# Kernel tuning notes

Hardware: AMD Instinct MI355X
Metric: run time of the kernel (lower is better)

## Reference

```python
import jax, jax.numpy as jnp
import numpy as np

ADMP = 16  # admp_channel


def _backbone(x, Wc, bc):
    # Conv2d(3->256, k=3, stride=2, pad=1) + ReLU stands in for feature_backbone
    y = jax.lax.conv_general_dilated(x, Wc, window_strides=(2, 2),
                                     padding=((1, 1), (1, 1)),
                                     dimension_numbers=('NCHW', 'OIHW', 'NCHW'))
    return jax.nn.relu(y + bc[None, :, None, None])


def _feature_select(feat, k):
    # AdaptiveMaxPool2d(k, return_indices=True) on feat.sum(1); H,W divisible by k
    B, C, H, W = feat.shape
    bh, bw = H // k, W // k
    resp = feat.sum(1)  # [B,H,W]
    r = resp.reshape(B, k, bh, k, bw).transpose(0, 1, 3, 2, 4).reshape(B, k, k, bh * bw)
    loc = jnp.argmax(r, axis=-1)            # local flat index in each bh*bw block
    lr, lc = loc // bw, loc % bw
    rows = jnp.arange(k)[None, :, None] * bh + lr   # [B,k,k]
    cols = jnp.arange(k)[None, None, :] * bw + lc
    return (rows * W + cols).reshape(B, k * k)      # flat indices into H*W


def _mlp(x, W1, b1, W2, b2):
    # Linear -> ReLU -> (Dropout eval = identity) -> Linear
    return jax.nn.relu(x @ W1 + b1) @ W2 + b2


def reference(xA, xB, Wconv, bconv, W1r, b1r, W2r, b2r, W1c, b1c, W2c, b2c):
    fA = _backbone(xA, Wconv, bconv)  # [B,C,H,W]
    fB = _backbone(xB, Wconv, bconv)
    B, C, H, W = fA.shape
    N = H * W
    idxA = _feature_select(fA, ADMP)                       # [B,K]
    fA_flat = fA.reshape(B, C, N)
    fB_flat = fB.reshape(B, C, N)
    desc = jnp.take_along_axis(fA_flat, idxA[:, None, :], axis=2)  # [B,C,K]
    # ||a-b||^2 = ||a||^2 - 2 a.b + ||b||^2 ; fused batched kNN
    dist = ((desc ** 2).sum(1)[:, :, None]
            - 2.0 * jnp.einsum('bck,bcn->bkn', desc, fB_flat)
            + (fB_flat ** 2).sum(1)[:, None, :])           # [B,K,N]
    minidx = jnp.argmin(dist, axis=-1)                     # [B,K]
    # original uses high (==width here since H==W) for both div and mod
    row_A, col_A = idxA // H, idxA % H
    row_B, col_B = minidx // H, minidx % H
    drow = (row_B - row_A).astype(jnp.float32)             # [B,K]
    dcol = (col_A - col_B).astype(jnp.float32)
    out_drow = _mlp(drow, W1r, b1r, W2r, b2r)              # [B,1]
    out_dcol = _mlp(dcol, W1c, b1c, W2c, b2c)
    return jnp.concatenate([out_drow, out_dcol], axis=1)   # [B,2]


def setup_inputs() -> dict:
    key = jax.random.key(0)
    ks = jax.random.split(key, 8)
    K2 = ADMP * ADMP
    return {
        'xA': jax.random.normal(ks[0], (4, 3, 256, 256), jnp.float32),
        'xB': jax.random.normal(ks[1], (4, 3, 256, 256), jnp.float32),
        'Wconv': jax.random.normal(ks[2], (256, 3, 3, 3), jnp.float32) * 0.1,
        'bconv': jnp.zeros((256,), jnp.float32),
        'W1r': jax.random.normal(ks[3], (K2, K2 // 2), jnp.float32) * 0.05,
        'b1r': jnp.zeros((K2 // 2,), jnp.float32),
        'W2r': jax.random.normal(ks[4], (K2 // 2, 1), jnp.float32) * 0.05,
        'b2r': jnp.zeros((1,), jnp.float32),
        'W1c': jax.random.normal(ks[5], (K2, K2 // 2), jnp.float32) * 0.05,
        'b1c': jnp.zeros((K2 // 2,), jnp.float32),
        'W2c': jax.random.normal(ks[6], (K2 // 2, 1), jnp.float32) * 0.05,
        'b2c': jnp.zeros((1,), jnp.float32),
    }
```

## Files before the change

### kernel.cpp

```cpp
#include <hip/hip_runtime.h>
#include <stdint.h>

constexpr int NB   = 4;
constexpr int CIN  = 3;
constexpr int HIN  = 256;
constexpr int COUT = 256;
constexpr int HF   = 128;
constexpr int NF   = HF * HF;
constexpr int KADM = 16;
constexpr int KK   = KADM * KADM;
constexpr int HID  = 128;
constexpr int DFB  = 65536;
constexpr int PX   = 64;
constexpr int NT   = NF / PX;

typedef unsigned short ushort_t;
typedef __attribute__((ext_vector_type(8))) _Float16 f16x8;
typedef __attribute__((ext_vector_type(2))) __fp16   fp16v2;
typedef __attribute__((ext_vector_type(4))) float    f32x4;

__device__ inline ushort_t f16bits(_Float16 h) { return __builtin_bit_cast(ushort_t, h); }

__device__ inline int swz(int pix, int c) {
    return pix * 256 + ((((c >> 3) ^ (pix & 7)) << 3) | (c & 7));
}

__device__ inline int dfoff(int kt, int chunk, int lane) {
    return ((kt * 8 + chunk) * 64 + lane) * 8;
}

__global__ __launch_bounds__(256) void prep_kernel(
        const float* __restrict__ W, ushort_t* __restrict__ WFh, ushort_t* __restrict__ WFl)
{
    int co = threadIdx.x;
    int kt = co >> 4, la = co & 15;
    #pragma unroll
    for (int q = 0; q < 32; ++q) {
        float v = (q < 27) ? W[co * 27 + q] : 0.f;
        _Float16 h = (_Float16)v;
        _Float16 l = (_Float16)(v - (float)h);
        int lg = q >> 3, e = q & 7;
        int off = (kt * 64 + lg * 16 + la) * 8 + e;
        WFh[off] = f16bits(h);
        WFl[off] = f16bits(l);
    }
}

__global__ __launch_bounds__(256) void convA_kernel(
        const float* __restrict__ xA,
        const ushort_t* __restrict__ WFh, const ushort_t* __restrict__ WFl,
        const float* __restrict__ bias, float* __restrict__ resp)
{
    __shared__ float    pS[CIN][3][132];
    __shared__ ushort_t Ah[64][40];
    __shared__ ushort_t Al[64][40];
    __shared__ float    redS[4][64];

    int tile = blockIdx.x;
    int b    = blockIdx.y;
    int oh   = tile >> 1;
    int ow0  = (tile & 1) << 6;
    const float* x = xA + (size_t)b * CIN * HIN * HIN;
    int tid = threadIdx.x;

    for (int i = tid; i < CIN * 3 * 129; i += 256) {
        int ci = i / (3 * 129);
        int r2 = i % (3 * 129);
        int kh = r2 / 129, c = r2 % 129;
        int gr = 2 * oh - 1 + kh, gc = 2 * ow0 - 1 + c;
        float v = 0.f;
        if (gr >= 0 && gr < HIN && gc >= 0 && gc < HIN)
            v = x[(size_t)ci * HIN * HIN + (size_t)gr * HIN + gc];
        pS[ci][kh][c] = v;
    }
    __syncthreads();

    {
        int n = tid >> 2, qg = tid & 3;
        unsigned uh[4], ul[4];
        #pragma unroll
        for (int e2 = 0; e2 < 4; ++e2) {
            ushort_t hh[2], ll[2];
            #pragma unroll
            for (int s = 0; s < 2; ++s) {
                int q = qg * 8 + e2 * 2 + s;
                float v = 0.f;
                if (q < 27) {
                    int ci = q / 9, r = (q % 9) / 3, kw = q % 3;
                    v = pS[ci][r][2 * n + kw];
                }
                _Float16 h = (_Float16)v;
                _Float16 l = (_Float16)(v - (float)h);
                hh[s] = f16bits(h); ll[s] = f16bits(l);
            }
            uh[e2] = (unsigned)hh[0] | ((unsigned)hh[1] << 16);
            ul[e2] = (unsigned)ll[0] | ((unsigned)ll[1] << 16);
        }
        *(uint4*)&Ah[n][qg * 8] = *(uint4*)uh;
        *(uint4*)&Al[n][qg * 8] = *(uint4*)ul;
    }
    __syncthreads();

    int lane = tid & 63, w = tid >> 6;
    int la = lane & 15, lg = lane >> 4;
    int wbase = w * 64;

    float bj[4];
    f16x8 bh[4], bl[4];
    #pragma unroll
    for (int j = 0; j < 4; ++j) {
        bj[j] = bias[wbase + j * 16 + la];
        int off = ((w * 4 + j) * 64 + lane) * 8;
        bh[j] = *(const f16x8*)&WFh[off];
        bl[j] = *(const f16x8*)&WFl[off];
    }

    f16x8 ah[4], al[4];
    #pragma unroll
    for (int i = 0; i < 4; ++i) {
        ah[i] = *(const f16x8*)&Ah[i * 16 + la][lg * 8];
        al[i] = *(const f16x8*)&Al[i * 16 + la][lg * 8];
    }

    f32x4 acc[4][4];
    #pragma unroll
    for (int i = 0; i < 4; ++i)
        #pragma unroll
        for (int j = 0; j < 4; ++j) acc[i][j] = (f32x4)0.f;

    #pragma unroll
    for (int i = 0; i < 4; ++i)
        #pragma unroll
        for (int j = 0; j < 4; ++j) {
            acc[i][j] = __builtin_amdgcn_mfma_f32_16x16x32_f16(ah[i], bh[j], acc[i][j], 0, 0, 0);
            acc[i][j] = __builtin_amdgcn_mfma_f32_16x16x32_f16(al[i], bh[j], acc[i][j], 0, 0, 0);
            acc[i][j] = __builtin_amdgcn_mfma_f32_16x16x32_f16(ah[i], bl[j], acc[i][j], 0, 0, 0);
        }

    float s[4][4];
    #pragma unroll
    for (int i = 0; i < 4; ++i)
        #pragma unroll
        for (int r = 0; r < 4; ++r) s[i][r] = 0.f;

    #pragma unroll
    for (int i = 0; i < 4; ++i)
        #pragma unroll
        for (int j = 0; j < 4; ++j)
            #pragma unroll
            for (int r = 0; r < 4; ++r)
                s[i][r] += fmaxf(acc[i][j][r] + bj[j], 0.f);

    #pragma unroll
    for (int i = 0; i < 4; ++i)
        #pragma unroll
        for (int r = 0; r < 4; ++r) {
            float v = s[i][r];
            v += __shfl_xor(v, 1, 64);
            v += __shfl_xor(v, 2, 64);
            v += __shfl_xor(v, 4, 64);
            v += __shfl_xor(v, 8, 64);
            s[i][r] = v;
        }
    if (la == 0) {
        #pragma unroll
        for (int i = 0; i < 4; ++i)
            #pragma unroll
            for (int r = 0; r < 4; ++r)
                redS[w][i * 16 + lg * 4 + r] = s[i][r];
    }
    __syncthreads();
    if (tid < 64) {
        float tot = redS[0][tid] + redS[1][tid] + redS[2][tid] + redS[3][tid];
        resp[(size_t)b * NF + oh * HF + ow0 + tid] = tot;
    }
}

__global__ __launch_bounds__(256) void select_kernel(
        const float* __restrict__ resp,
        const float* __restrict__ xA, const float* __restrict__ W,
        const float* __restrict__ bias,
        int* __restrict__ idxA,
        ushort_t* __restrict__ dFh, ushort_t* __restrict__ dFl,
        float* __restrict__ normA)
{
    __shared__ float patch[27];
    __shared__ float red[4];
    __shared__ int   sidx;

    int bk = blockIdx.x;
    int b = bk >> 8, k = bk & 255;
    int t = threadIdx.x;

    if (t < 64) {
        int kr = k >> 4, kc = k & 15;
        int lr = t >> 3, lc = t & 7;
        int row = kr * 8 + lr, col = kc * 8 + lc;
        float bv = resp[(size_t)b * NF + (size_t)row * HF + col];
        int best = t;
        for (int off = 32; off > 0; off >>= 1) {
            float ov = __shfl_down(bv, off, 64);
            int   oi = __shfl_down(best, off, 64);
            if (ov > bv || (ov == bv && oi < best)) { bv = ov; best = oi; }
        }
        if (t == 0) {
            int r = kr * 8 + (best >> 3), c = kc * 8 + (best & 7);
            int idx = r * HF + c;
            idxA[bk] = idx;
            sidx = idx;
        }
    }
    __syncthreads();
    int idx = sidx;
    int oh = idx >> 7, ow = idx & 127;

    if (t < 27) {
        int ci = t / 9, kh = (t % 9) / 3, kw = t % 3;
        int ir = oh * 2 - 1 + kh, ic = ow * 2 - 1 + kw;
        float v = 0.f;
        if (ir >= 0 && ir < HIN && ic >= 0 && ic < HIN)
            v = xA[((size_t)b * CIN + ci) * HIN * HIN + (size_t)ir * HIN + ic];
        patch[t] = v;
    }
    __syncthreads();

    float v = bias[t];
    const float* w = &W[t * 27];
    #pragma unroll
    for (int q = 0; q < 27; ++q) v = fmaf(patch[q], w[q], v);
    v = fmaxf(v, 0.f);

    _Float16 h = (_Float16)v;
    _Float16 l = (_Float16)(v - (float)h);
    {
        int kt = k >> 4, la = k & 15;
        int chunk = t >> 5, lg = (t >> 3) & 3, e = t & 7;
        int off = b * DFB + dfoff(kt, chunk, lg * 16 + la) + e;
        dFh[off] = f16bits(h);
        dFl[off] = f16bits(l);
    }

    float s = v * v;
    for (int off = 32; off > 0; off >>= 1) s += __shfl_down(s, off, 64);
    if ((t & 63) == 0) red[t >> 6] = s;
    __syncthreads();
    if (t == 0) normA[bk] = red[0] + red[1] + red[2] + red[3];
}

__device__ inline void load_desc(const ushort_t* __restrict__ dFh,
                                 const ushort_t* __restrict__ dFl,
                                 int w, int chunk, int lane,
                                 f16x8* bh, f16x8* bl)
{
    #pragma unroll
    for (int jj = 0; jj < 2; ++jj) {
        int off = dfoff(w * 2 + jj, chunk, lane);
        bh[jj] = *(const f16x8*)&dFh[off];
        bl[jj] = *(const f16x8*)&dFl[off];
    }
}

__device__ inline void knn_chunk(const ushort_t* __restrict__ fH,
                                 const ushort_t* __restrict__ fL,
                                 int la, int lg, int cc,
                                 const f16x8* bh, const f16x8* bl,
                                 f32x4 (&acc)[4][2])
{
    #pragma unroll
    for (int i = 0; i < 4; ++i) {
        f16x8 ah = *(const f16x8*)&fH[swz(i * 16 + la, cc + lg * 8)];
        f16x8 al = *(const f16x8*)&fL[swz(i * 16 + la, cc + lg * 8)];
        __builtin_amdgcn_s_setprio(1);
        #pragma unroll
        for (int jj = 0; jj < 2; ++jj) {
            acc[i][jj] = __builtin_amdgcn_mfma_f32_16x16x32_f16(ah, bh[jj], acc[i][jj], 0, 0, 0);
            acc[i][jj] = __builtin_amdgcn_mfma_f32_16x16x32_f16(al, bh[jj], acc[i][jj], 0, 0, 0);
            acc[i][jj] = __builtin_amdgcn_mfma_f32_16x16x32_f16(ah, bl[jj], acc[i][jj], 0, 0, 0);
        }
        __builtin_amdgcn_s_setprio(0);
    }
}

__global__ __launch_bounds__(512, 4) void fused_kernel(
        const float* __restrict__ xB,
        const ushort_t* __restrict__ WFh, const ushort_t* __restrict__ WFl,
        const float* __restrict__ bias,
        const ushort_t* __restrict__ dFhg, const ushort_t* __restrict__ dFlg,
        const float* __restrict__ normA,
        unsigned long long* __restrict__ packed)
{
    __shared__ __align__(16) char smem[2 * PX * 256 * 2];
    __shared__ float redS[8][PX];
    __shared__ float nAS[KK];
    __shared__ float nBS[PX];
    __shared__ float bS[COUT];

    float*    pSp = (float*)smem;
    ushort_t* AhP = (ushort_t*)(smem + 4752);
    ushort_t* AlP = (ushort_t*)(smem + 4752 + 5120);
    ushort_t* fH  = (ushort_t*)smem;
    ushort_t* fL  = (ushort_t*)(smem + PX * 256 * 2);

    int tile = blockIdx.x;
    int b    = blockIdx.y;
    int oh   = tile >> 1;
    int ow0  = (tile & 1) << 6;
    const float* x = xB + (size_t)b * CIN * HIN * HIN;
    int tid = threadIdx.x;

    if (tid < KK) {
        nAS[tid] = normA[b * KK + tid];
        bS[tid]  = bias[tid];
    }

    for (int i = tid; i < CIN * 3 * 129; i += 512) {
        int ci = i / (3 * 129);
        int r2 = i % (3 * 129);
        int kh = r2 / 129, c = r2 % 129;
        int gr = 2 * oh - 1 + kh, gc = 2 * ow0 - 1 + c;
        float v = 0.f;
        if (gr >= 0 && gr < HIN && gc >= 0 && gc < HIN)
            v = x[(size_t)ci * HIN * HIN + (size_t)gr * HIN + gc];
        pSp[ci * 396 + kh * 132 + c] = v;
    }
    __syncthreads();

    {
        int n = tid >> 3, qg = tid & 7;
        ushort_t hh[4], ll[4];
        #pragma unroll
        for (int s = 0; s < 4; ++s) {
            int q = qg * 4 + s;
            float v = 0.f;
            if (q < 27) {
                int ci = q / 9, r = (q % 9) / 3, kw = q % 3;
                v = pSp[ci * 396 + r * 132 + 2 * n + kw];
            }
            _Float16 h = (_Float16)v;
            _Float16 l = (_Float16)(v - (float)h);
            hh[s] = f16bits(h); ll[s] = f16bits(l);
        }
        unsigned lo, hi;
        lo = (unsigned)hh[0] | ((unsigned)hh[1] << 16);
        hi = (unsigned)hh[2] | ((unsigned)hh[3] << 16);
        *(uint2*)&AhP[n * 40 + qg * 4] = make_uint2(lo, hi);
        lo = (unsigned)ll[0] | ((unsigned)ll[1] << 16);
        hi = (unsigned)ll[2] | ((unsigned)ll[3] << 16);
        *(uint2*)&AlP[n * 40 + qg * 4] = make_uint2(lo, hi);
    }
    __syncthreads();

    int lane = tid & 63, w = tid >> 6;
    int la = lane & 15, lg = lane >> 4;

    f16x8 wah[2], wal[2], pbh[4], pbl[4];
    #pragma unroll
    for (int jj = 0; jj < 2; ++jj) {
        int off = ((w * 2 + jj) * 64 + lane) * 8;
        wah[jj] = *(const f16x8*)&WFh[off];
        wal[jj] = *(const f16x8*)&WFl[off];
    }
    #pragma unroll
    for (int i = 0; i < 4; ++i) {
        pbh[i] = *(const f16x8*)&AhP[(i * 16 + la) * 40 + lg * 8];
        pbl[i] = *(const f16x8*)&AlP[(i * 16 + la) * 40 + lg * 8];
    }

    f32x4 cacc[2][4];
    #pragma unroll
    for (int jj = 0; jj < 2; ++jj)
        #pragma unroll
        for (int i = 0; i < 4; ++i) cacc[jj][i] = (f32x4)0.f;

    #pragma unroll
    for (int jj = 0; jj < 2; ++jj)
        #pragma unroll
        for (int i = 0; i < 4; ++i) {
            cacc[jj][i] = __builtin_amdgcn_mfma_f32_16x16x32_f16(wah[jj], pbh[i], cacc[jj][i], 0, 0, 0);
            cacc[jj][i] = __builtin_amdgcn_mfma_f32_16x16x32_f16(wal[jj], pbh[i], cacc[jj][i], 0, 0, 0);
            cacc[jj][i] = __builtin_amdgcn_mfma_f32_16x16x32_f16(wah[jj], pbl[i], cacc[jj][i], 0, 0, 0);
        }

    __syncthreads();

    float s2[4] = {0.f, 0.f, 0.f, 0.f};
    #pragma unroll
    for (int jj = 0; jj < 2; ++jj) {
        int co4 = (w * 2 + jj) * 16 + lg * 4;
        f32x4 b4 = *(const f32x4*)&bS[co4];
        int chunk = co4 >> 3;
        int within = (lg & 1) * 4;
        #pragma unroll
        for (int i = 0; i < 4; ++i) {
            int pix = i * 16 + la;
            float v0 = fmaxf(cacc[jj][i][0] + b4[0], 0.f);
            float v1 = fmaxf(cacc[jj][i][1] + b4[1], 0.f);
            float v2 = fmaxf(cacc[jj][i][2] + b4[2], 0.f);
            float v3 = fmaxf(cacc[jj][i][3] + b4[3], 0.f);
            s2[i] += v0 * v0 + v1 * v1 + v2 * v2 + v3 * v3;
            fp16v2 h01 = __builtin_amdgcn_cvt_pkrtz(v0, v1);
            fp16v2 h23 = __builtin_amdgcn_cvt_pkrtz(v2, v3);
            fp16v2 l01 = __builtin_amdgcn_cvt_pkrtz(v0 - (float)h01[0], v1 - (float)h01[1]);
            fp16v2 l23 = __builtin_amdgcn_cvt_pkrtz(v2 - (float)h23[0], v3 - (float)h23[1]);
            int base = pix * 256 + ((chunk ^ (pix & 7)) << 3) + within;
            *(uint2*)&fH[base] = make_uint2(__builtin_bit_cast(unsigned, h01),
                                            __builtin_bit_cast(unsigned, h23));
            *(uint2*)&fL[base] = make_uint2(__builtin_bit_cast(unsigned, l01),
                                            __builtin_bit_cast(unsigned, l23));
        }
    }

    const ushort_t* dFh = dFhg + (size_t)b * DFB;
    const ushort_t* dFl = dFlg + (size_t)b * DFB;
    f16x8 bhA[2], blA[2], bhB[2], blB[2];
    load_desc(dFh, dFl, w, 0, lane, bhA, blA);
    load_desc(dFh, dFl, w, 1, lane, bhB, blB);

    #pragma unroll
    for (int i = 0; i < 4; ++i) {
        float v = s2[i];
        v += __shfl_xor(v, 16, 64);
        v += __shfl_xor(v, 32, 64);
        if (lg == 0) redS[w][i * 16 + la] = v;
    }
    __syncthreads();
    if (tid < PX) {
        float t0 = 0.f;
        #pragma unroll
        for (int p = 0; p < 8; ++p) t0 += redS[p][tid];
        nBS[tid] = t0;
    }
    __syncthreads();

    f32x4 acc[4][2];
    #pragma unroll
    for (int i = 0; i < 4; ++i)
        #pragma unroll
        for (int jj = 0; jj < 2; ++jj) acc[i][jj] = (f32x4)0.f;

    knn_chunk(fH, fL, la, lg, 0, bhA, blA, acc);
    load_desc(dFh, dFl, w, 2, lane, bhA, blA);
    knn_chunk(fH, fL, la, lg, 32, bhB, blB, acc);
    load_desc(dFh, dFl, w, 3, lane, bhB, blB);
    knn_chunk(fH, fL, la, lg, 64, bhA, blA, acc);
    load_desc(dFh, dFl, w, 4, lane, bhA, blA);
    knn_chunk(fH, fL, la, lg, 96, bhB, blB, acc);
    load_desc(dFh, dFl, w, 5, lane, bhB, blB);
    knn_chunk(fH, fL, la, lg, 128, bhA, blA, acc);
    load_desc(dFh, dFl, w, 6, lane, bhA, blA);
    knn_chunk(fH, fL, la, lg, 160, bhB, blB, acc);
    load_desc(dFh, dFl, w, 7, lane, bhB, blB);
    knn_chunk(fH, fL, la, lg, 192, bhA, blA, acc);
    knn_chunk(fH, fL, la, lg, 224, bhB, blB, acc);

    float nBv[4][4];
    #pragma unroll
    for (int i = 0; i < 4; ++i) {
        f32x4 t4 = *(const f32x4*)&nBS[i * 16 + lg * 4];
        nBv[i][0] = t4[0]; nBv[i][1] = t4[1]; nBv[i][2] = t4[2]; nBv[i][3] = t4[3];
    }
    int n0 = tile * PX;
    float bd[2];
    int   bn[2];
    #pragma unroll
    for (int jj = 0; jj < 2; ++jj) {
        int kl = (w * 2 + jj) * 16 + la;
        float nAv = nAS[kl];
        float bestd = 3.4e38f;
        int   bestn = 0;
        #pragma unroll
        for (int i = 0; i < 4; ++i)
            #pragma unroll
            for (int r = 0; r < 4; ++r) {
                int n = n0 + i * 16 + lg * 4 + r;
                float d = fmaf(-2.f, acc[i][jj][r], nAv) + nBv[i][r];
                if (d < bestd) { bestd = d; bestn = n; }
            }
        #pragma unroll
        for (int off = 16; off <= 32; off <<= 1) {
            float od = __shfl_xor(bestd, off, 64);
            int   on = __shfl_xor(bestn, off, 64);
            bool take = (od < bestd) || (od == bestd && on < bestn);
            bestd = take ? od : bestd;
            bestn = take ? on : bestn;
        }
        bd[jj] = bestd; bn[jj] = bestn;
    }
    if (lg < 2) {
        float fd = (lg == 0) ? bd[0] : bd[1];
        int   fn = (lg == 0) ? bn[0] : bn[1];
        unsigned u = __float_as_uint(fd);
        u = (u & 0x80000000u) ? ~u : (u | 0x80000000u);
        unsigned long long key = ((unsigned long long)u << 32) | (unsigned)fn;
        int klw = (w * 2 + lg) * 16 + la;
        atomicMin(&packed[b * KK + klw], key);
    }
}

__global__ __launch_bounds__(128) void mlp_kernel(
        const int* __restrict__ idxA, const unsigned long long* __restrict__ packed,
        const float* __restrict__ W1r, const float* __restrict__ b1r,
        const float* __restrict__ W2r, const float* __restrict__ b2r,
        const float* __restrict__ W1c, const float* __restrict__ b1c,
        const float* __restrict__ W2c, const float* __restrict__ b2c,
        float* __restrict__ out)
{
    __shared__ float xS[KK];
    __shared__ float red[2];
    int blk = blockIdx.x;
    int b = blk >> 1, which = blk & 1;
    int t = threadIdx.x;

    for (int k = t; k < KK; k += 128) {
        int ia = idxA[b * KK + k];
        int nn = (int)(packed[b * KK + k] & 0xffffffffULL);
        int rowA = ia >> 7, colA = ia & 127;
        int rowB = nn >> 7, colB = nn & 127;
        xS[k] = (which == 0) ? (float)(rowB - rowA) : (float)(colA - colB);
    }
    __syncthreads();

    const float* W1 = which ? W1c : W1r;
    const float* b1 = which ? b1c : b1r;
    const float* W2 = which ? W2c : W2r;
    const float* b2 = which ? b2c : b2r;

    float h = b1[t];
    for (int k = 0; k < KK; ++k) h = fmaf(xS[k], W1[k * HID + t], h);
    h = fmaxf(h, 0.f);
    float pv = h * W2[t];
    for (int off = 32; off > 0; off >>= 1) pv += __shfl_down(pv, off, 64);
    if ((t & 63) == 0) red[t >> 6] = pv;
    __syncthreads();
    if (t == 0) out[b * 2 + which] = red[0] + red[1] + b2[0];
}

extern "C" void kernel_launch(void* const* d_in, const int* in_sizes, int n_in,
                              void* d_out, int out_size, void* d_ws, size_t ws_size,
                              hipStream_t stream)
{
    const float* xA  = (const float*)d_in[0];
    const float* xB  = (const float*)d_in[1];
    const float* Wc  = (const float*)d_in[2];
    const float* bc  = (const float*)d_in[3];
    const float* W1r = (const float*)d_in[4];
    const float* b1r = (const float*)d_in[5];
    const float* W2r = (const float*)d_in[6];
    const float* b2r = (const float*)d_in[7];
    const float* W1c = (const float*)d_in[8];
    const float* b1c = (const float*)d_in[9];
    const float* W2c = (const float*)d_in[10];
    const float* b2c = (const float*)d_in[11];
    float* out = (float*)d_out;

    char* ws = (char*)d_ws;
    unsigned long long* packed = (unsigned long long*)ws; ws += (size_t)NB * KK * 8;
    int*   idxA   = (int*)ws;      ws += (size_t)NB * KK * 4;
    float* normA  = (float*)ws;    ws += (size_t)NB * KK * 4;
    float* resp   = (float*)ws;    ws += (size_t)NB * NF * 4;
    ushort_t* dFh = (ushort_t*)ws; ws += (size_t)NB * DFB * 2;
    ushort_t* dFl = (ushort_t*)ws; ws += (size_t)NB * DFB * 2;
    ushort_t* WFh = (ushort_t*)ws; ws += (size_t)COUT * 32 * 2;
    ushort_t* WFl = (ushort_t*)ws; ws += (size_t)COUT * 32 * 2;

    hipMemsetAsync(packed, 0xFF, (size_t)NB * KK * 8, stream);

    prep_kernel  <<<1, 256, 0, stream>>>(Wc, WFh, WFl);
    convA_kernel <<<dim3(256, NB), 256, 0, stream>>>(xA, WFh, WFl, bc, resp);
    select_kernel<<<NB * KK, 256, 0, stream>>>(resp, xA, Wc, bc, idxA, dFh, dFl, normA);
    fused_kernel <<<dim3(NT, NB), 512, 0, stream>>>(xB, WFh, WFl, bc, dFh, dFl,
                                                    normA, packed);
    mlp_kernel   <<<8, 128, 0, stream>>>(idxA, packed,
                                         W1r, b1r, W2r, b2r,
                                         W1c, b1c, W2c, b2c, out);
}
```

Baseline: 60.26 us.

## Widen fused conv+kNN tile to full 128-pixel row with 1024-thread blocks

Each fused block now processes a full output row of 128 pixels using 16 waves, and each wave owns 16 descriptor columns instead of 32. The patch staging covers the full input row width, and the per-wave accumulators are reorganised as 8 pixel subtiles by 1 descriptor tile. This halves the block count and the per-block redundant loads of descriptors, norms and bias, and gives one atomic per descriptor per block. In exchange it doubles the shared memory per block and uses larger blocks, which may reduce occupancy or leave the GPU underfilled, since only 512 blocks are launched.

```diff
diff --git a/kernel.cpp b/kernel.cpp
--- a/kernel.cpp
+++ b/kernel.cpp
@@ -11,7 +11,7 @@
 constexpr int KK   = KADM * KADM;
 constexpr int HID  = 128;
 constexpr int DFB  = 65536;
-constexpr int PX   = 64;
+constexpr int PX   = 128;
 constexpr int NT   = NF / PX;
 
 typedef unsigned short ushort_t;
@@ -249,39 +249,33 @@
 
 __device__ inline void load_desc(const ushort_t* __restrict__ dFh,
                                  const ushort_t* __restrict__ dFl,
-                                 int w, int chunk, int lane,
-                                 f16x8* bh, f16x8* bl)
-{
-    #pragma unroll
-    for (int jj = 0; jj < 2; ++jj) {
-        int off = dfoff(w * 2 + jj, chunk, lane);
-        bh[jj] = *(const f16x8*)&dFh[off];
-        bl[jj] = *(const f16x8*)&dFl[off];
-    }
+                                 int kt, int chunk, int lane,
+                                 f16x8& bh, f16x8& bl)
+{
+    int off = dfoff(kt, chunk, lane);
+    bh = *(const f16x8*)&dFh[off];
+    bl = *(const f16x8*)&dFl[off];
 }
 
 __device__ inline void knn_chunk(const ushort_t* __restrict__ fH,
                                  const ushort_t* __restrict__ fL,
                                  int la, int lg, int cc,
-                                 const f16x8* bh, const f16x8* bl,
-                                 f32x4 (&acc)[4][2])
-{
-    #pragma unroll
-    for (int i = 0; i < 4; ++i) {
+                                 f16x8 bh, f16x8 bl,
+                                 f32x4 (&acc)[8])
+{
+    #pragma unroll
+    for (int i = 0; i < 8; ++i) {
         f16x8 ah = *(const f16x8*)&fH[swz(i * 16 + la, cc + lg * 8)];
         f16x8 al = *(const f16x8*)&fL[swz(i * 16 + la, cc + lg * 8)];
         __builtin_amdgcn_s_setprio(1);
-        #pragma unroll
-        for (int jj = 0; jj < 2; ++jj) {
-            acc[i][jj] = __builtin_amdgcn_mfma_f32_16x16x32_f16(ah, bh[jj], acc[i][jj], 0, 0, 0);
-            acc[i][jj] = __builtin_amdgcn_mfma_f32_16x16x32_f16(al, bh[jj], acc[i][jj], 0, 0, 0);
-            acc[i][jj] = __builtin_amdgcn_mfma_f32_16x16x32_f16(ah, bl[jj], acc[i][jj], 0, 0, 0);
-        }
+        acc[i] = __builtin_amdgcn_mfma_f32_16x16x32_f16(ah, bh, acc[i], 0, 0, 0);
+        acc[i] = __builtin_amdgcn_mfma_f32_16x16x32_f16(al, bh, acc[i], 0, 0, 0);
+        acc[i] = __builtin_amdgcn_mfma_f32_16x16x32_f16(ah, bl, acc[i], 0, 0, 0);
         __builtin_amdgcn_s_setprio(0);
     }
 }
 
-__global__ __launch_bounds__(512, 4) void fused_kernel(
+__global__ __launch_bounds__(1024, 4) void fused_kernel(
         const float* __restrict__ xB,
         const ushort_t* __restrict__ WFh, const ushort_t* __restrict__ WFl,
         const float* __restrict__ bias,
@@ -290,21 +284,19 @@
         unsigned long long* __restrict__ packed)
 {
     __shared__ __align__(16) char smem[2 * PX * 256 * 2];
-    __shared__ float redS[8][PX];
+    __shared__ float redS[16][PX];
     __shared__ float nAS[KK];
     __shared__ float nBS[PX];
     __shared__ float bS[COUT];
 
     float*    pSp = (float*)smem;
-    ushort_t* AhP = (ushort_t*)(smem + 4752);
-    ushort_t* AlP = (ushort_t*)(smem + 4752 + 5120);
+    ushort_t* AhP = (ushort_t*)(smem + 9360);
+    ushort_t* AlP = (ushort_t*)(smem + 9360 + 10240);
     ushort_t* fH  = (ushort_t*)smem;
     ushort_t* fL  = (ushort_t*)(smem + PX * 256 * 2);
 
-    int tile = blockIdx.x;
-    int b    = blockIdx.y;
-    int oh   = tile >> 1;
-    int ow0  = (tile & 1) << 6;
+    int oh = blockIdx.x;
+    int b  = blockIdx.y;
     const float* x = xB + (size_t)b * CIN * HIN * HIN;
     int tid = threadIdx.x;
 
@@ -313,15 +305,15 @@
         bS[tid]  = bias[tid];
     }
 
-    for (int i = tid; i < CIN * 3 * 129; i += 512) {
-        int ci = i / (3 * 129);
-        int r2 = i % (3 * 129);
-        int kh = r2 / 129, c = r2 % 129;
-        int gr = 2 * oh - 1 + kh, gc = 2 * ow0 - 1 + c;
+    for (int i = tid; i < CIN * 3 * 258; i += 1024) {
+        int ci = i / (3 * 258);
+        int r2 = i % (3 * 258);
+        int kh = r2 / 258, c = r2 % 258;
+        int gr = 2 * oh - 1 + kh, gc = c - 1;
         float v = 0.f;
         if (gr >= 0 && gr < HIN && gc >= 0 && gc < HIN)
             v = x[(size_t)ci * HIN * HIN + (size_t)gr * HIN + gc];
-        pSp[ci * 396 + kh * 132 + c] = v;
+        pSp[ci * 780 + kh * 260 + c] = v;
     }
     __syncthreads();
 
@@ -334,7 +326,7 @@
             float v = 0.f;
             if (q < 27) {
                 int ci = q / 9, r = (q % 9) / 3, kw = q % 3;
-                v = pSp[ci * 396 + r * 132 + 2 * n + kw];
+                v = pSp[ci * 780 + r * 260 + 2 * n + kw];
             }
             _Float16 h = (_Float16)v;
             _Float16 l = (_Float16)(v - (float)h);
@@ -353,71 +345,60 @@
     int lane = tid & 63, w = tid >> 6;
     int la = lane & 15, lg = lane >> 4;
 
-    f16x8 wah[2], wal[2], pbh[4], pbl[4];
-    #pragma unroll
-    for (int jj = 0; jj < 2; ++jj) {
-        int off = ((w * 2 + jj) * 64 + lane) * 8;
-        wah[jj] = *(const f16x8*)&WFh[off];
-        wal[jj] = *(const f16x8*)&WFl[off];
-    }
-    #pragma unroll
-    for (int i = 0; i < 4; ++i) {
-        pbh[i] = *(const f16x8*)&AhP[(i * 16 + la) * 40 + lg * 8];
-        pbl[i] = *(const f16x8*)&AlP[(i * 16 + la) * 40 + lg * 8];
-    }
-
-    f32x4 cacc[2][4];
-    #pragma unroll
-    for (int jj = 0; jj < 2; ++jj)
-        #pragma unroll
-        for (int i = 0; i < 4; ++i) cacc[jj][i] = (f32x4)0.f;
-
-    #pragma unroll
-    for (int jj = 0; jj < 2; ++jj)
-        #pragma unroll
-        for (int i = 0; i < 4; ++i) {
-            cacc[jj][i] = __builtin_amdgcn_mfma_f32_16x16x32_f16(wah[jj], pbh[i], cacc[jj][i], 0, 0, 0);
-            cacc[jj][i] = __builtin_amdgcn_mfma_f32_16x16x32_f16(wal[jj], pbh[i], cacc[jj][i], 0, 0, 0);
-            cacc[jj][i] = __builtin_amdgcn_mfma_f32_16x16x32_f16(wah[jj], pbl[i], cacc[jj][i], 0, 0, 0);
-        }
-
-    __syncthreads();
-
-    float s2[4] = {0.f, 0.f, 0.f, 0.f};
-    #pragma unroll
-    for (int jj = 0; jj < 2; ++jj) {
-        int co4 = (w * 2 + jj) * 16 + lg * 4;
-        f32x4 b4 = *(const f32x4*)&bS[co4];
-        int chunk = co4 >> 3;
-        int within = (lg & 1) * 4;
-        #pragma unroll
-        for (int i = 0; i < 4; ++i) {
-            int pix = i * 16 + la;
-            float v0 = fmaxf(cacc[jj][i][0] + b4[0], 0.f);
-            float v1 = fmaxf(cacc[jj][i][1] + b4[1], 0.f);
-            float v2 = fmaxf(cacc[jj][i][2] + b4[2], 0.f);
-            float v3 = fmaxf(cacc[jj][i][3] + b4[3], 0.f);
-            s2[i] += v0 * v0 + v1 * v1 + v2 * v2 + v3 * v3;
-            fp16v2 h01 = __builtin_amdgcn_cvt_pkrtz(v0, v1);
-            fp16v2 h23 = __builtin_amdgcn_cvt_pkrtz(v2, v3);
-            fp16v2 l01 = __builtin_amdgcn_cvt_pkrtz(v0 - (float)h01[0], v1 - (float)h01[1]);
-            fp16v2 l23 = __builtin_amdgcn_cvt_pkrtz(v2 - (float)h23[0], v3 - (float)h23[1]);
-            int base = pix * 256 + ((chunk ^ (pix & 7)) << 3) + within;
-            *(uint2*)&fH[base] = make_uint2(__builtin_bit_cast(unsigned, h01),
-                                            __builtin_bit_cast(unsigned, h23));
-            *(uint2*)&fL[base] = make_uint2(__builtin_bit_cast(unsigned, l01),
-                                            __builtin_bit_cast(unsigned, l23));
-        }
+    f16x8 wah, wal;
+    {
+        int off = (w * 64 + lane) * 8;
+        wah = *(const f16x8*)&WFh[off];
+        wal = *(const f16x8*)&WFl[off];
+    }
+
+    f32x4 cacc[8];
+    #pragma unroll
+    for (int i = 0; i < 8; ++i) cacc[i] = (f32x4)0.f;
+
+    #pragma unroll
+    for (int i = 0; i < 8; ++i) {
+        f16x8 pbh = *(const f16x8*)&AhP[(i * 16 + la) * 40 + lg * 8];
+        f16x8 pbl = *(const f16x8*)&AlP[(i * 16 + la) * 40 + lg * 8];
+        cacc[i] = __builtin_amdgcn_mfma_f32_16x16x32_f16(wah, pbh, cacc[i], 0, 0, 0);
+        cacc[i] = __builtin_amdgcn_mfma_f32_16x16x32_f16(wal, pbh, cacc[i], 0, 0, 0);
+        cacc[i] = __builtin_amdgcn_mfma_f32_16x16x32_f16(wah, pbl, cacc[i], 0, 0, 0);
+    }
+
+    __syncthreads();
+
+    int co4 = w * 16 + lg * 4;
+    f32x4 b4 = *(const f32x4*)&bS[co4];
+    int chunk0 = co4 >> 3;
+    int within = (lg & 1) * 4;
+    float s2[8];
+    #pragma unroll
+    for (int i = 0; i < 8; ++i) {
+        int pix = i * 16 + la;
+        float v0 = fmaxf(cacc[i][0] + b4[0], 0.f);
+        float v1 = fmaxf(cacc[i][1] + b4[1], 0.f);
+        float v2 = fmaxf(cacc[i][2] + b4[2], 0.f);
+        float v3 = fmaxf(cacc[i][3] + b4[3], 0.f);
+        s2[i] = v0 * v0 + v1 * v1 + v2 * v2 + v3 * v3;
+        fp16v2 h01 = __builtin_amdgcn_cvt_pkrtz(v0, v1);
+        fp16v2 h23 = __builtin_amdgcn_cvt_pkrtz(v2, v3);
+        fp16v2 l01 = __builtin_amdgcn_cvt_pkrtz(v0 - (float)h01[0], v1 - (float)h01[1]);
+        fp16v2 l23 = __builtin_amdgcn_cvt_pkrtz(v2 - (float)h23[0], v3 - (float)h23[1]);
+        int base = pix * 256 + ((chunk0 ^ (pix & 7)) << 3) + within;
+        *(uint2*)&fH[base] = make_uint2(__builtin_bit_cast(unsigned, h01),
+                                        __builtin_bit_cast(unsigned, h23));
+        *(uint2*)&fL[base] = make_uint2(__builtin_bit_cast(unsigned, l01),
+                                        __builtin_bit_cast(unsigned, l23));
     }
 
     const ushort_t* dFh = dFhg + (size_t)b * DFB;
     const ushort_t* dFl = dFlg + (size_t)b * DFB;
-    f16x8 bhA[2], blA[2], bhB[2], blB[2];
+    f16x8 bhA, blA, bhB, blB;
     load_desc(dFh, dFl, w, 0, lane, bhA, blA);
     load_desc(dFh, dFl, w, 1, lane, bhB, blB);
 
     #pragma unroll
-    for (int i = 0; i < 4; ++i) {
+    for (int i = 0; i < 8; ++i) {
         float v = s2[i];
         v += __shfl_xor(v, 16, 64);
         v += __shfl_xor(v, 32, 64);
@@ -427,16 +408,14 @@
     if (tid < PX) {
         float t0 = 0.f;
         #pragma unroll
-        for (int p = 0; p < 8; ++p) t0 += redS[p][tid];
+        for (int p = 0; p < 16; ++p) t0 += redS[p][tid];
         nBS[tid] = t0;
     }
     __syncthreads();
 
-    f32x4 acc[4][2];
-    #pragma unroll
-    for (int i = 0; i < 4; ++i)
-        #pragma unroll
-        for (int jj = 0; jj < 2; ++jj) acc[i][jj] = (f32x4)0.f;
+    f32x4 acc[8];
+    #pragma unroll
+    for (int i = 0; i < 8; ++i) acc[i] = (f32x4)0.f;
 
     knn_chunk(fH, fL, la, lg, 0, bhA, blA, acc);
     load_desc(dFh, dFl, w, 2, lane, bhA, blA);
@@ -453,47 +432,33 @@
     knn_chunk(fH, fL, la, lg, 192, bhA, blA, acc);
     knn_chunk(fH, fL, la, lg, 224, bhB, blB, acc);
 
-    float nBv[4][4];
-    #pragma unroll
-    for (int i = 0; i < 4; ++i) {
+    int n0 = oh * PX;
+    float nAv = nAS[w * 16 + la];
+    float bestd = 3.4e38f;
+    int   bestn = 0;
+    #pragma unroll
+    for (int i = 0; i < 8; ++i) {
         f32x4 t4 = *(const f32x4*)&nBS[i * 16 + lg * 4];
-        nBv[i][0] = t4[0]; nBv[i][1] = t4[1]; nBv[i][2] = t4[2]; nBv[i][3] = t4[3];
-    }
-    int n0 = tile * PX;
-    float bd[2];
-    int   bn[2];
-    #pragma unroll
-    for (int jj = 0; jj < 2; ++jj) {
-        int kl = (w * 2 + jj) * 16 + la;
-        float nAv = nAS[kl];
-        float bestd = 3.4e38f;
-        int   bestn = 0;
-        #pragma unroll
-        for (int i = 0; i < 4; ++i)
-            #pragma unroll
-            for (int r = 0; r < 4; ++r) {
-                int n = n0 + i * 16 + lg * 4 + r;
-                float d = fmaf(-2.f, acc[i][jj][r], nAv) + nBv[i][r];
-                if (d < bestd) { bestd = d; bestn = n; }
-            }
-        #pragma unroll
-        for (int off = 16; off <= 32; off <<= 1) {
-            float od = __shfl_xor(bestd, off, 64);
-            int   on = __shfl_xor(bestn, off, 64);
-            bool take = (od < bestd) || (od == bestd && on < bestn);
-            bestd = take ? od : bestd;
-            bestn = take ? on : bestn;
-        }
-        bd[jj] = bestd; bn[jj] = bestn;
-    }
-    if (lg < 2) {
-        float fd = (lg == 0) ? bd[0] : bd[1];
-        int   fn = (lg == 0) ? bn[0] : bn[1];
-        unsigned u = __float_as_uint(fd);
+        #pragma unroll
+        for (int r = 0; r < 4; ++r) {
+            int n = n0 + i * 16 + lg * 4 + r;
+            float d = fmaf(-2.f, acc[i][r], nAv) + t4[r];
+            if (d < bestd) { bestd = d; bestn = n; }
+        }
+    }
+    #pragma unroll
+    for (int off = 16; off <= 32; off <<= 1) {
+        float od = __shfl_xor(bestd, off, 64);
+        int   on = __shfl_xor(bestn, off, 64);
+        bool take = (od < bestd) || (od == bestd && on < bestn);
+        bestd = take ? od : bestd;
+        bestn = take ? on : bestn;
+    }
+    if (lg == 0) {
+        unsigned u = __float_as_uint(bestd);
         u = (u & 0x80000000u) ? ~u : (u | 0x80000000u);
-        unsigned long long key = ((unsigned long long)u << 32) | (unsigned)fn;
-        int klw = (w * 2 + lg) * 16 + la;
-        atomicMin(&packed[b * KK + klw], key);
+        unsigned long long key = ((unsigned long long)u << 32) | (unsigned)bestn;
+        atomicMin(&packed[b * KK + w * 16 + la], key);
     }
 }
 
@@ -568,8 +533,8 @@
     prep_kernel  <<<1, 256, 0, stream>>>(Wc, WFh, WFl);
     convA_kernel <<<dim3(256, NB), 256, 0, stream>>>(xA, WFh, WFl, bc, resp);
     select_kernel<<<NB * KK, 256, 0, stream>>>(resp, xA, Wc, bc, idxA, dFh, dFl, normA);
-    fused_kernel <<<dim3(NT, NB), 512, 0, stream>>>(xB, WFh, WFl, bc, dFh, dFl,
-                                                    normA, packed);
+    fused_kernel <<<dim3(NT, NB), 1024, 0, stream>>>(xB, WFh, WFl, bc, dFh, dFl,
+                                                     normA, packed);
     mlp_kernel   <<<8, 128, 0, stream>>>(idxA, packed,
                                          W1r, b1r, W2r, b2r,
                                          W1c, b1c, W2c, b2c, out);
```

New measurement: 62.00 us. +2.9%, slower.
